# Kernel tuning notes

Hardware: AMD Instinct MI355X
Metric: run time of the kernel (lower is better)

Reference implementation:

```python
import jax, jax.numpy as jnp
import numpy as np

B, L, D, V = 4096, 200, 64, 100000
ATTR_LEN = (2, 6, 10)  # label_size = 18
NEG = -1e9


def setup_inputs() -> dict:
    key = jax.random.key(0)
    ks = jax.random.split(key, 12)
    x = jax.random.randint(ks[0], (B, L), 0, V)
    lengths = jax.random.randint(ks[1], (B,), 1, L + 1)  # ragged valid lengths >= 1
    x_mask = jnp.arange(L)[None, :] < lengths[:, None]   # prefix-valid bool mask [B,L]
    y = (jax.random.uniform(ks[2], (B, sum(ATTR_LEN))) < 0.5).astype(jnp.float32)
    ob = (jax.random.uniform(ks[3], (B, sum(ATTR_LEN))) < 0.8).astype(jnp.float32)
    emb_table = (jax.random.normal(ks[4], (V, D)) * 0.02).at[0].set(0.0)  # padding_idx=0
    tran_W = jax.random.normal(ks[5], (3, D, D)) * 0.05   # emb_tran Linear weights (per attr)
    tran_b = jnp.zeros((3, D))
    att_W = jax.random.normal(ks[6], (3, D)) * 0.05       # item_att_W: Linear(D,1) per attr
    att_b = jnp.zeros((3,))
    W0 = jax.random.normal(ks[7], (D, ATTR_LEN[0])) * 0.05  # W_all (no bias)
    W1 = jax.random.normal(ks[8], (D, ATTR_LEN[1])) * 0.05
    W2 = jax.random.normal(ks[9], (D, ATTR_LEN[2])) * 0.05
    return {"x": x, "x_mask": x_mask, "y": y, "ob": ob, "emb_table": emb_table,
            "tran_W": tran_W, "tran_b": tran_b, "att_W": att_W, "att_b": att_b,
            "W0": W0, "W1": W1, "W2": W2}


def reference(x, x_mask, y, ob, emb_table, tran_W, tran_b, att_W, att_b, W0, W1, W2):
    # embed: [B,L,D]
    embed = emb_table[x]
    # per-attribute transformed embeddings: [3,B,L,D]
    e = jax.nn.relu(jnp.einsum('bld,ade->able', embed, tran_W) + tran_b[:, None, None, :])
    # attention logits per attribute: [3,B,L]
    att_u = jax.nn.relu(jnp.einsum('able,ae->abl', e, att_W) + att_b[:, None, None])
    # masked softmax over valid prefix (equivalent to the per-sample length loop)
    m = x_mask.astype(e.dtype)
    scores = jnp.where(x_mask[None, :, :], att_u, NEG)
    att = jax.nn.softmax(scores, axis=-1) * m[None, :, :]
    # attention-pooled user representation per attribute: [3,B,D]
    rep = jnp.tanh(jnp.einsum('abl,able->abe', att, e))
    # torch: cat([rep_a.unsqueeze(2)],2).view(B,-1) -> interleaved (d-major, attr-minor) layout
    user_flat = jnp.transpose(rep, (1, 2, 0)).reshape(rep.shape[1], -1)  # [B, 3*D]
    Ddim = emb_table.shape[1]
    W_user = jnp.concatenate([user_flat[:, 0 * Ddim:1 * Ddim] @ W0,
                              user_flat[:, 1 * Ddim:2 * Ddim] @ W1,
                              user_flat[:, 2 * Ddim:3 * Ddim] @ W2], axis=1)
    # W_compact = W_user * ob  (observed-label mask)
    return W_user * ob
```

## Files before the change

kernel.cpp:

```cpp
#include <hip/hip_runtime.h>

typedef unsigned int u32;
typedef unsigned short u16;
typedef unsigned char u8;
typedef unsigned long long u64;

typedef __attribute__((ext_vector_type(8))) short bf16x8;
typedef __attribute__((ext_vector_type(4))) float f32x4;

#define L_SEQ 200

__device__ __forceinline__ u16 f2bf(float f) {
    u32 u = __float_as_uint(f);
    return (u16)((u + 0x7FFFu + ((u >> 16) & 1u)) >> 16);
}
__device__ __forceinline__ u32 pk2bf(float fx, float fy) {
    u32 xb = __float_as_uint(fx) + 0x8000u;
    u32 yb = __float_as_uint(fy) + 0x8000u;
    return __byte_perm(xb, yb, 0x7632);
}
__device__ __forceinline__ float wave_sumf(float v) {
#pragma unroll
    for (int off = 32; off; off >>= 1) v += __shfl_xor(v, off, 64);
    return v;
}

__global__ __launch_bounds__(256) void etna_prep(const void* __restrict__ xmask,
                                                 const float* __restrict__ tranW,
                                                 const float* __restrict__ emb,
                                                 void* __restrict__ ws, int Bn, int Vn) {
    const int tid = threadIdx.x;
    const int bid = blockIdx.x;

    {
        u64* dst = (u64*)((char*)ws + 40960);
        const float4* src = (const float4*)emb;
        int ng = Vn * 16;
        for (int i = bid * 256 + tid; i < ng; i += gridDim.x * 256) {
            float4 v = src[i];
            u64 lo = pk2bf(v.x, v.y);
            u64 hi = pk2bf(v.z, v.w);
            dst[i] = lo | (hi << 32);
        }
    }

    if (bid < 48) {
        int it = bid * 256 + tid;
        int jj = it & 7;
        int ln = (it >> 3) & 63;
        int kh = (it >> 9) & 1;
        int c = (it >> 10) & 3;
        int a = it >> 12;
        int k = kh * 32 + (ln >> 4) * 8 + jj;
        int n = c * 16 + (ln & 15);
        ((u16*)ws)[it] = f2bf(tranW[a * 4096 + k * 64 + n]);
        return;
    }

    const int wv = tid >> 6;
    const int lane = tid & 63;
    int esz;
    {
        u32 accF = 0, acc0 = 0, accO = 0;
#pragma unroll
        for (int k = 0; k < 4; ++k) {
            int i = lane + 64 * k;
            u32 w = (i < 200) ? ((const u32*)xmask)[i] : 0u;
            accF |= (w & 0xFEFEFEFEu);
            acc0 |= (w & 0x000000FFu);
            accO |= (w & 0xFFFFFF00u);
        }
        bool isFloat = __ballot(accF != 0) != 0;
        bool hasB0   = __ballot(acc0 != 0) != 0;
        bool hasOdd  = __ballot(accO != 0) != 0;
        esz = isFloat ? (hasB0 ? 2 : 4) : (hasOdd ? 1 : 4);
    }
    int s = (bid - 48) * 4 + wv;
    if (s < Bn) {
        int len = 0;
        int mbase = s * L_SEQ;
#pragma unroll
        for (int c4 = 0; c4 < 4; ++c4) {
            int l = c4 * 64 + lane;
            bool v = false;
            if (l < L_SEQ) {
                int off = mbase + l;
                if (esz == 1)      v = ((const u8*)xmask)[off] != 0;
                else if (esz == 2) v = ((const u16*)xmask)[off] != 0;
                else               v = ((const u32*)xmask)[off] != 0;
            }
            len += (int)__popcll(__ballot(v));
        }
        if (lane == 0) ((int*)((char*)ws + 24576))[s] = len;
    }
}

__global__ __launch_bounds__(192, 4) void etna_mfma(
    const int* __restrict__ x, const float* __restrict__ ob,
    const float* __restrict__ tranb, const float* __restrict__ attW,
    const float* __restrict__ attb, const float* __restrict__ W0,
    const float* __restrict__ W1, const float* __restrict__ W2,
    float* __restrict__ out, const void* __restrict__ ws, int Vn) {
    __shared__ float repl[3][64];

    const int tid = threadIdx.x;
    const int a = tid >> 6;
    const int lane = tid & 63;
    const int col = lane & 15;
    const int g = lane >> 4;
    const int b = blockIdx.x;

    const u16* wsBf = (const u16*)ws;
    bf16x8 Bf[4][2];
#pragma unroll
    for (int c = 0; c < 4; ++c)
#pragma unroll
        for (int kh = 0; kh < 2; ++kh)
            Bf[c][kh] = *(const bf16x8*)&wsBf[(((a * 4 + c) * 2 + kh) * 64 + lane) * 8];

    const int len = ((const int*)((const char*)ws + 24576))[b];
    const u16* wsEmb = (const u16*)((const char*)ws + 40960);

    const float LOG2E = 1.44269504088896f;
    float TB[4], AW[4];
#pragma unroll
    for (int c = 0; c < 4; ++c) {
        TB[c] = tranb[a * 64 + c * 16 + col];
        AW[c] = attW[a * 64 + c * 16 + col] * LOG2E;
    }
    const float AB = attb[a] * LOG2E;

    const int* xrow = x + b * L_SEQ;
    int iv[4];
#pragma unroll
    for (int c4 = 0; c4 < 4; ++c4) {
        int l = c4 * 64 + lane;
        int id = (l < L_SEQ) ? xrow[l] : 0;
        iv[c4] = max(0, min(id, Vn - 1));
    }

    float NUM[4] = {0.f, 0.f, 0.f, 0.f};
    float DEN = 0.f;
    const int ntiles = (len + 15) >> 4;

    bf16x8 a0, a1, n0, n1;
    {
        int p = col;
        int id = __shfl(iv[0], p, 64);
        id = (p < len) ? id : 0;
        const bf16x8* rp = (const bf16x8*)(wsEmb + (size_t)id * 64);
        a0 = rp[g];
        a1 = rp[4 + g];
    }

    for (int t = 0; t < ntiles; ++t) {
        n0 = a0; n1 = a1;
        if (t + 1 < ntiles) {
            int p = (t + 1) * 16 + col;
            int id = __shfl(iv[p >> 6], p & 63, 64);
            id = (p < len) ? id : 0;
            const bf16x8* rn = (const bf16x8*)(wsEmb + (size_t)id * 64);
            n0 = rn[g];
            n1 = rn[4 + g];
        }
        const int l0 = t << 4;

        f32x4 E[4];
#pragma unroll
        for (int c = 0; c < 4; ++c) {
            f32x4 cc = {TB[c], TB[c], TB[c], TB[c]};
            cc = __builtin_amdgcn_mfma_f32_16x16x32_bf16(a0, Bf[c][0], cc, 0, 0, 0);
            cc = __builtin_amdgcn_mfma_f32_16x16x32_bf16(a1, Bf[c][1], cc, 0, 0, 0);
            E[c].x = fmaxf(cc.x, 0.f);
            E[c].y = fmaxf(cc.y, 0.f);
            E[c].z = fmaxf(cc.z, 0.f);
            E[c].w = fmaxf(cc.w, 0.f);
        }
        float p0 = E[0].x * AW[0] + E[1].x * AW[1] + E[2].x * AW[2] + E[3].x * AW[3];
        float p1 = E[0].y * AW[0] + E[1].y * AW[1] + E[2].y * AW[2] + E[3].y * AW[3];
        float p2 = E[0].z * AW[0] + E[1].z * AW[1] + E[2].z * AW[2] + E[3].z * AW[3];
        float p3 = E[0].w * AW[0] + E[1].w * AW[1] + E[2].w * AW[2] + E[3].w * AW[3];
#pragma unroll
        for (int off = 1; off <= 8; off <<= 1) {
            p0 += __shfl_xor(p0, off, 64);
            p1 += __shfl_xor(p1, off, 64);
            p2 += __shfl_xor(p2, off, 64);
            p3 += __shfl_xor(p3, off, 64);
        }
        int lrow = l0 + 4 * g;
        float u0 = fmaxf(p0 + AB, 0.f);
        float u1 = fmaxf(p1 + AB, 0.f);
        float u2 = fmaxf(p2 + AB, 0.f);
        float u3 = fmaxf(p3 + AB, 0.f);
        float s0 = (lrow + 0 < len) ? exp2f(u0) : 0.f;
        float s1 = (lrow + 1 < len) ? exp2f(u1) : 0.f;
        float s2 = (lrow + 2 < len) ? exp2f(u2) : 0.f;
        float s3 = (lrow + 3 < len) ? exp2f(u3) : 0.f;
        DEN += s0 + s1 + s2 + s3;
#pragma unroll
        for (int c = 0; c < 4; ++c)
            NUM[c] += s0 * E[c].x + s1 * E[c].y + s2 * E[c].z + s3 * E[c].w;

        a0 = n0;
        a1 = n1;
    }

    {
        float d = DEN;
        d += __shfl_xor(d, 16, 64);
        d += __shfl_xor(d, 32, 64);
        float rden = 1.0f / fmaxf(d, 1e-20f);
#pragma unroll
        for (int c = 0; c < 4; ++c) {
            float v = NUM[c];
            v += __shfl_xor(v, 16, 64);
            v += __shfl_xor(v, 32, 64);
            if (g == 0) repl[a][c * 16 + col] = tanhf(v * rden);
        }
    }
    __syncthreads();

    if (a == 0) {
        float outv = 0.f;
        {
            int gg = lane; float v = repl[gg % 3][gg / 3];
#pragma unroll
            for (int k = 0; k < 2; ++k) {
                float p = wave_sumf(v * W0[lane * 2 + k]);
                if (lane == k) outv = p;
            }
        }
        {
            int gg = 64 + lane; float v = repl[gg % 3][gg / 3];
#pragma unroll
            for (int k = 0; k < 6; ++k) {
                float p = wave_sumf(v * W1[lane * 6 + k]);
                if (lane == 2 + k) outv = p;
            }
        }
        {
            int gg = 128 + lane; float v = repl[gg % 3][gg / 3];
#pragma unroll
            for (int k = 0; k < 10; ++k) {
                float p = wave_sumf(v * W2[lane * 10 + k]);
                if (lane == 8 + k) outv = p;
            }
        }
        if (lane < 18) out[b * 18 + lane] = outv * ob[b * 18 + lane];
    }
}

extern "C" void kernel_launch(void* const* d_in, const int* in_sizes, int n_in,
                              void* d_out, int out_size, void* d_ws, size_t ws_size,
                              hipStream_t stream) {
    const int* x = (const int*)d_in[0];
    const void* xmask = d_in[1];
    const float* ob = (const float*)d_in[3];
    const float* emb = (const float*)d_in[4];
    const float* tranW = (const float*)d_in[5];
    const float* tranb = (const float*)d_in[6];
    const float* attW = (const float*)d_in[7];
    const float* attb = (const float*)d_in[8];
    const float* W0 = (const float*)d_in[9];
    const float* W1 = (const float*)d_in[10];
    const float* W2 = (const float*)d_in[11];

    const int Bn = in_sizes[0] / L_SEQ;
    const int Vn = in_sizes[4] / 64;

    etna_prep<<<48 + (Bn + 3) / 4, 256, 0, stream>>>(xmask, tranW, emb, d_ws, Bn, Vn);
    etna_mfma<<<Bn, 192, 0, stream>>>(x, ob, tranb, attW, attb,
                                      W0, W1, W2, (float*)d_out, d_ws, Vn);
}
```

Before: 138.1 us.

## Split fused attention kernel into per-attribute wave blocks plus separate epilogue kernel

```diff
diff --git a/kernel.cpp b/kernel.cpp
--- a/kernel.cpp
+++ b/kernel.cpp
@@ -95,20 +95,16 @@
     }
 }
 
-__global__ __launch_bounds__(192, 4) void etna_mfma(
-    const int* __restrict__ x, const float* __restrict__ ob,
-    const float* __restrict__ tranb, const float* __restrict__ attW,
-    const float* __restrict__ attb, const float* __restrict__ W0,
-    const float* __restrict__ W1, const float* __restrict__ W2,
-    float* __restrict__ out, const void* __restrict__ ws, int Vn) {
-    __shared__ float repl[3][64];
-
-    const int tid = threadIdx.x;
-    const int a = tid >> 6;
-    const int lane = tid & 63;
+__global__ __launch_bounds__(64) void etna_attn(
+    const int* __restrict__ x, const float* __restrict__ tranb,
+    const float* __restrict__ attW, const float* __restrict__ attb,
+    void* __restrict__ ws, int Vn) {
+    const int bid = blockIdx.x;
+    const int s = bid / 3;
+    const int a = bid - s * 3;
+    const int lane = threadIdx.x;
     const int col = lane & 15;
     const int g = lane >> 4;
-    const int b = blockIdx.x;
 
     const u16* wsBf = (const u16*)ws;
     bf16x8 Bf[4][2];
@@ -118,7 +114,7 @@
         for (int kh = 0; kh < 2; ++kh)
             Bf[c][kh] = *(const bf16x8*)&wsBf[(((a * 4 + c) * 2 + kh) * 64 + lane) * 8];
 
-    const int len = ((const int*)((const char*)ws + 24576))[b];
+    const int len = ((const int*)((const char*)ws + 24576))[s];
     const u16* wsEmb = (const u16*)((const char*)ws + 40960);
 
     const float LOG2E = 1.44269504088896f;
@@ -130,7 +126,7 @@
     }
     const float AB = attb[a] * LOG2E;
 
-    const int* xrow = x + b * L_SEQ;
+    const int* xrow = x + s * L_SEQ;
     int iv[4];
 #pragma unroll
     for (int c4 = 0; c4 < 4; ++c4) {
@@ -205,6 +201,7 @@
         a1 = n1;
     }
 
+    float* wsRep = (float*)((char*)ws + 40960 + (size_t)Vn * 128);
     {
         float d = DEN;
         d += __shfl_xor(d, 16, 64);
@@ -215,39 +212,52 @@
             float v = NUM[c];
             v += __shfl_xor(v, 16, 64);
             v += __shfl_xor(v, 32, 64);
-            if (g == 0) repl[a][c * 16 + col] = tanhf(v * rden);
-        }
-    }
-    __syncthreads();
-
-    if (a == 0) {
-        float outv = 0.f;
-        {
-            int gg = lane; float v = repl[gg % 3][gg / 3];
-#pragma unroll
-            for (int k = 0; k < 2; ++k) {
-                float p = wave_sumf(v * W0[lane * 2 + k]);
-                if (lane == k) outv = p;
-            }
-        }
-        {
-            int gg = 64 + lane; float v = repl[gg % 3][gg / 3];
-#pragma unroll
-            for (int k = 0; k < 6; ++k) {
-                float p = wave_sumf(v * W1[lane * 6 + k]);
-                if (lane == 2 + k) outv = p;
-            }
-        }
-        {
-            int gg = 128 + lane; float v = repl[gg % 3][gg / 3];
-#pragma unroll
-            for (int k = 0; k < 10; ++k) {
-                float p = wave_sumf(v * W2[lane * 10 + k]);
-                if (lane == 8 + k) outv = p;
-            }
-        }
-        if (lane < 18) out[b * 18 + lane] = outv * ob[b * 18 + lane];
-    }
+            if (g == 0) wsRep[(size_t)s * 192 + a * 64 + c * 16 + col] = tanhf(v * rden);
+        }
+    }
+}
+
+__global__ __launch_bounds__(256) void etna_epi(
+    const float* __restrict__ ob, const float* __restrict__ W0,
+    const float* __restrict__ W1, const float* __restrict__ W2,
+    float* __restrict__ out, const void* __restrict__ ws, int Vn) {
+    __shared__ float repl[4][3][64];
+    const int tid = threadIdx.x;
+    const int wv = tid >> 6;
+    const int lane = tid & 63;
+    const int s = blockIdx.x * 4 + wv;
+
+    const float* wsRep = (const float*)((const char*)ws + 40960 + (size_t)Vn * 128);
+#pragma unroll
+    for (int a = 0; a < 3; ++a)
+        repl[wv][a][lane] = wsRep[(size_t)s * 192 + a * 64 + lane];
+
+    float outv = 0.f;
+    {
+        int gg = lane; float v = repl[wv][gg % 3][gg / 3];
+#pragma unroll
+        for (int k = 0; k < 2; ++k) {
+            float p = wave_sumf(v * W0[lane * 2 + k]);
+            if (lane == k) outv = p;
+        }
+    }
+    {
+        int gg = 64 + lane; float v = repl[wv][gg % 3][gg / 3];
+#pragma unroll
+        for (int k = 0; k < 6; ++k) {
+            float p = wave_sumf(v * W1[lane * 6 + k]);
+            if (lane == 2 + k) outv = p;
+        }
+    }
+    {
+        int gg = 128 + lane; float v = repl[wv][gg % 3][gg / 3];
+#pragma unroll
+        for (int k = 0; k < 10; ++k) {
+            float p = wave_sumf(v * W2[lane * 10 + k]);
+            if (lane == 8 + k) outv = p;
+        }
+    }
+    if (lane < 18) out[s * 18 + lane] = outv * ob[s * 18 + lane];
 }
 
 extern "C" void kernel_launch(void* const* d_in, const int* in_sizes, int n_in,
@@ -269,6 +279,6 @@
     const int Vn = in_sizes[4] / 64;
 
     etna_prep<<<48 + (Bn + 3) / 4, 256, 0, stream>>>(xmask, tranW, emb, d_ws, Bn, Vn);
-    etna_mfma<<<Bn, 192, 0, stream>>>(x, ob, tranb, attW, attb,
-                                      W0, W1, W2, (float*)d_out, d_ws, Vn);
-}
+    etna_attn<<<Bn * 3, 64, 0, stream>>>(x, tranb, attW, attb, d_ws, Vn);
+    etna_epi<<<(Bn + 3) / 4, 256, 0, stream>>>(ob, W0, W1, W2, (float*)d_out, d_ws, Vn);
+}
```

New measurement: 140.6 us. No clear change (+1.8%).
